# Kernel optimization log

Hardware: AMD Instinct MI355X
Metric: run time of the kernel (lower is better)

Reference implementation:

```python
import jax, jax.numpy as jnp
import numpy as np

WS = 8          # window size
SS = 4          # shift size
NH = 4          # num heads
DIM = 128
RPE_HID = 512
MLP_HID = 512   # 4 * DIM
EPS = 1e-5


def _rel_coords_table(ws):
    h = np.arange(-(ws - 1), ws, dtype=np.float32)
    tbl = np.stack(np.meshgrid(h, h, indexing='ij'), axis=-1)  # [2ws-1, 2ws-1, 2]
    tbl = tbl / (ws - 1) * 8.0
    tbl = np.sign(tbl) * np.log2(np.abs(tbl) + 1.0) / np.log2(8.0)
    return jnp.asarray(tbl, dtype=jnp.float32)


def _rel_pos_index(ws):
    coords = np.stack(np.meshgrid(np.arange(ws), np.arange(ws), indexing='ij'))  # [2, ws, ws]
    cf = coords.reshape(2, -1)
    rel = (cf[:, :, None] - cf[:, None, :]).transpose(1, 2, 0).astype(np.int64)  # [N, N, 2]
    rel[..., 0] += ws - 1
    rel[..., 1] += ws - 1
    rel[..., 0] *= 2 * ws - 1
    return jnp.asarray(rel.sum(-1))  # [N, N]


def _attn_mask(H, W, ws, ss):
    img = np.zeros((H, W), np.float32)
    cnt = 0
    for hsl in (slice(0, -ws), slice(-ws, -ss), slice(-ss, None)):
        for wsl in (slice(0, -ws), slice(-ws, -ss), slice(-ss, None)):
            img[hsl, wsl] = cnt
            cnt += 1
    mw = img.reshape(H // ws, ws, W // ws, ws).transpose(0, 2, 1, 3).reshape(-1, ws * ws)
    diff = mw[:, None, :] - mw[:, :, None]
    return jnp.asarray(np.where(diff != 0, -100.0, 0.0).astype(np.float32))  # [nW, N, N]


def _layernorm(x, w, b):
    mu = x.mean(-1, keepdims=True)
    var = ((x - mu) ** 2).mean(-1, keepdims=True)
    return (x - mu) * jax.lax.rsqrt(var + EPS) * w + b


def setup_inputs() -> dict:
    key = jax.random.key(0)
    ks = jax.random.split(key, 16)
    s = 0.02
    return {
        'x': jax.random.normal(ks[0], (32, 4096, DIM), jnp.float32),
        'qkv_w': jax.random.normal(ks[1], (3 * DIM, DIM), jnp.float32) * s,
        'qkv_b': jnp.zeros((3 * DIM,), jnp.float32),
        'proj_w': jax.random.normal(ks[2], (DIM, DIM), jnp.float32) * s,
        'proj_b': jnp.zeros((DIM,), jnp.float32),
        'rpe_w1': jax.random.normal(ks[3], (RPE_HID, 2), jnp.float32) * s,
        'rpe_b1': jnp.zeros((RPE_HID,), jnp.float32),
        'rpe_w2': jax.random.normal(ks[4], (NH, RPE_HID), jnp.float32) * s,
        'norm1_w': jnp.ones((DIM,), jnp.float32),
        'norm1_b': jnp.zeros((DIM,), jnp.float32),
        'fc1_w': jax.random.normal(ks[5], (MLP_HID, DIM), jnp.float32) * s,
        'fc1_b': jnp.zeros((MLP_HID,), jnp.float32),
        'fc2_w': jax.random.normal(ks[6], (DIM, MLP_HID), jnp.float32) * s,
        'fc2_b': jnp.zeros((DIM,), jnp.float32),
        'norm2_w': jnp.ones((DIM,), jnp.float32),
        'norm2_b': jnp.zeros((DIM,), jnp.float32),
        'H': 64,
        'W': 64,
    }


def reference(x, qkv_w, qkv_b, proj_w, proj_b, rpe_w1, rpe_b1, rpe_w2,
              norm1_w, norm1_b, fc1_w, fc1_b, fc2_w, fc2_b, norm2_w, norm2_b, H, W):
    B, L, C = x.shape
    N = WS * WS
    hd = C // NH
    scale = hd ** -0.5
    nWh, nWw = H // WS, W // WS
    nW = nWh * nWw

    # ---- shifted window partition ----
    xs = x.reshape(B, H, W, C)
    xs = jnp.roll(xs, shift=(-SS, -SS), axis=(1, 2))
    xw = xs.reshape(B, nWh, WS, nWw, WS, C).transpose(0, 1, 3, 2, 4, 5).reshape(-1, N, C)

    # ---- window attention ----
    qkv = xw @ qkv_w.T + qkv_b                              # [B*nW, N, 3C]
    qkv = qkv.reshape(-1, N, 3, NH, hd).transpose(2, 0, 3, 1, 4)
    q, k, v = qkv[0], qkv[1], qkv[2]                        # [B*nW, NH, N, hd]
    attn = jnp.einsum('whnd,whmd->whnm', q * scale, k)      # [B*nW, NH, N, N]

    # continuous relative position bias via MLP on log-spaced coords
    tbl = _rel_coords_table(WS)                             # [2ws-1, 2ws-1, 2]
    t = jax.nn.relu(tbl @ rpe_w1.T + rpe_b1) @ rpe_w2.T     # [2ws-1, 2ws-1, NH]
    t = t.reshape(-1, NH)
    rel_idx = _rel_pos_index(WS)                            # [N, N]
    bias = t[rel_idx].transpose(2, 0, 1)                    # [NH, N, N]
    attn = attn + bias[None]

    # shift mask
    mask = _attn_mask(H, W, WS, SS)                         # [nW, N, N]
    attn = attn.reshape(B, nW, NH, N, N) + mask[None, :, None]
    attn = jax.nn.softmax(attn, axis=-1).reshape(-1, NH, N, N)

    out = jnp.einsum('whnm,whmd->whnd', attn, v)            # [B*nW, NH, N, hd]
    out = out.transpose(0, 2, 1, 3).reshape(-1, N, C)
    out = out @ proj_w.T + proj_b

    # ---- window reverse + unshift ----
    out = out.reshape(B, nWh, nWw, WS, WS, C).transpose(0, 1, 3, 2, 4, 5).reshape(B, H, W, C)
    out = jnp.roll(out, shift=(SS, SS), axis=(1, 2)).reshape(B, L, C)

    # ---- post-norm residual ----
    x = x + _layernorm(out, norm1_w, norm1_b)

    # ---- MLP (GELU exact) + post-norm residual ----
    h = jax.nn.gelu(x @ fc1_w.T + fc1_b, approximate=False)
    h = h @ fc2_w.T + fc2_b
    x = x + _layernorm(h, norm2_w, norm2_b)
    return x
```

## Files before the change

### kernel.cpp

```cpp
#include <hip/hip_runtime.h>
#include <hip/hip_bf16.h>

typedef __attribute__((ext_vector_type(8))) short short8_t;
typedef __attribute__((ext_vector_type(4))) float f32x4_t;
typedef __attribute__((ext_vector_type(2))) float f32x2_t;

#define NHEAD 4
#define SCALE 0.17677669529663687f

#define OFF_W    0L
#define OFF_TBL  393216L
#define OFF_QKV  458752L
#define OFF_H    458752L
#define OFF_ATTN 101122048L
#define OFF_X1BF 134676480L

__device__ __forceinline__ unsigned short f2bf(float f){
  unsigned int u = __float_as_uint(f);
  u += 0x7FFFu + ((u >> 16) & 1u);
  return (unsigned short)(u >> 16);
}
__device__ __forceinline__ float bf2f(unsigned short s){
  return __uint_as_float(((unsigned int)s) << 16);
}

__device__ __forceinline__ int win_row_to_orig(int r){
  int win = r >> 6, n = r & 63;
  int b = win >> 6, wh = (win >> 3) & 7, ww = win & 7;
  int hs = wh*8 + (n >> 3), wsv = ww*8 + (n & 7);
  return (b << 12) + (((hs + 4) & 63) << 6) + ((wsv + 4) & 63);
}

__device__ __forceinline__ float gelu_exact(float x){
  float z  = x * 0.70710678118654752f;
  float az = fabsf(z);
  float t  = __builtin_amdgcn_rcpf(1.0f + 0.3275911f * az);
  float poly = t*(0.254829592f + t*(-0.284496736f + t*(1.421413741f +
               t*(-1.453152027f + t*1.061405429f))));
  float er = 1.0f - poly * __expf(-z*z);
  er = (z < 0.f) ? -er : er;
  return 0.5f * x * (1.0f + er);
}

__global__ __launch_bounds__(256) void prep_kernel(
    const float* __restrict__ qkv_w, const float* __restrict__ proj_w,
    const float* __restrict__ fc1_w, const float* __restrict__ fc2_w,
    const float* __restrict__ rpe_w1, const float* __restrict__ rpe_b1,
    const float* __restrict__ rpe_w2,
    unsigned short* __restrict__ wbf, float* __restrict__ tbl)
{
  if (blockIdx.x == 0) {
    int t = threadIdx.x;
    if (t < 225) {
      int a = t / 15, b = t % 15;
      float v0 = (float)(a - 7) * (8.0f / 7.0f);
      float v1 = (float)(b - 7) * (8.0f / 7.0f);
      float c0 = (v0 > 0.f ? 1.f : (v0 < 0.f ? -1.f : 0.f)) * log2f(fabsf(v0) + 1.f) * (1.0f/3.0f);
      float c1 = (v1 > 0.f ? 1.f : (v1 < 0.f ? -1.f : 0.f)) * log2f(fabsf(v1) + 1.f) * (1.0f/3.0f);
      float a0 = 0.f, a1 = 0.f, a2 = 0.f, a3 = 0.f;
      for (int k = 0; k < 512; k++){
        float h = c0 * rpe_w1[2*k] + c1 * rpe_w1[2*k+1] + rpe_b1[k];
        h = fmaxf(h, 0.f);
        a0 += h * rpe_w2[k];
        a1 += h * rpe_w2[512 + k];
        a2 += h * rpe_w2[1024 + k];
        a3 += h * rpe_w2[1536 + k];
      }
      tbl[t] = a0; tbl[225 + t] = a1; tbl[450 + t] = a2; tbl[675 + t] = a3;
    }
  } else {
    int e = (blockIdx.x - 1) * 256 + threadIdx.x;
    float v;
    if (e < 49152)       v = qkv_w[e];
    else if (e < 65536)  v = proj_w[e - 49152];
    else if (e < 131072) v = fc1_w[e - 65536];
    else                 v = fc2_w[e - 131072];
    wbf[e] = f2bf(v);
  }
}

template<int N, int AMODE, int EPI>
__global__ __launch_bounds__(256) void gemm_a_kernel(
    const void* __restrict__ Ap, const unsigned short* __restrict__ Bw,
    const float* __restrict__ bias, unsigned short* __restrict__ Out)
{
  constexpr int K  = 128;
  constexpr int NC = N / 32;
  int lane = threadIdx.x & 63;
  int wave = threadIdx.x >> 6;
  int l15 = lane & 15, kg = lane >> 4;
  int m0 = (blockIdx.x * 4 + wave) * 64;

  short8_t a[4][4];
#pragma unroll
  for (int mr = 0; mr < 4; mr++){
    int r = m0 + mr*16 + l15;
    if (AMODE == 1) r = win_row_to_orig(r);
    if (AMODE == 2){
      const unsigned short* ap = (const unsigned short*)Ap + (long)r * K + kg * 8;
#pragma unroll
      for (int kc = 0; kc < 4; kc++)
        a[mr][kc] = *(const short8_t*)(ap + kc * 32);
    } else {
      const float* ap = (const float*)Ap + (long)r * K + kg * 8;
#pragma unroll
      for (int kc = 0; kc < 4; kc++){
        f32x4_t a0 = *(const f32x4_t*)(ap + kc * 32);
        f32x4_t a1 = *(const f32x4_t*)(ap + kc * 32 + 4);
        union { short8_t v; unsigned short u[8]; } pk;
        pk.u[0] = f2bf(a0[0]); pk.u[1] = f2bf(a0[1]); pk.u[2] = f2bf(a0[2]); pk.u[3] = f2bf(a0[3]);
        pk.u[4] = f2bf(a1[0]); pk.u[5] = f2bf(a1[1]); pk.u[6] = f2bf(a1[2]); pk.u[7] = f2bf(a1[3]);
        a[mr][kc] = pk.v;
      }
    }
  }

  const unsigned short* bp0 = Bw + (long)l15 * K + kg * 8;

#pragma unroll 2
  for (int nc = 0; nc < NC; nc++){
    short8_t b[2][4];
#pragma unroll
    for (int nr = 0; nr < 2; nr++)
#pragma unroll
      for (int kc = 0; kc < 4; kc++)
        b[nr][kc] = *(const short8_t*)(bp0 + (long)(nc*32 + nr*16) * K + kc * 32);

    f32x4_t acc[4][2];
#pragma unroll
    for (int mr = 0; mr < 4; mr++)
#pragma unroll
      for (int nr = 0; nr < 2; nr++) acc[mr][nr] = (f32x4_t){0.f,0.f,0.f,0.f};
#pragma unroll
    for (int kc = 0; kc < 4; kc++)
#pragma unroll
      for (int mr = 0; mr < 4; mr++)
#pragma unroll
        for (int nr = 0; nr < 2; nr++)
          acc[mr][nr] = __builtin_amdgcn_mfma_f32_16x16x32_bf16(a[mr][kc], b[nr][kc], acc[mr][nr], 0, 0, 0);

#pragma unroll
    for (int nr = 0; nr < 2; nr++){
      int col = nc*32 + nr*16 + l15;
      float bv = bias[col];
#pragma unroll
      for (int mr = 0; mr < 4; mr++)
#pragma unroll
        for (int i = 0; i < 4; i++){
          float v = acc[mr][nr][i] + bv;
          if (EPI == 2) v = gelu_exact(v);
          Out[(long)(m0 + mr*16 + kg*4 + i) * N + col] = f2bf(v);
        }
    }
  }
}

template<int K, int SCATTER, int RESBF, int OUTBF>
__global__ __launch_bounds__(256) void gemm_b_ln_kernel(
    const unsigned short* __restrict__ Ap, const unsigned short* __restrict__ Bw,
    const float* __restrict__ bias,
    const float* __restrict__ lnw, const float* __restrict__ lnb,
    const void* __restrict__ Res, void* __restrict__ OutP)
{
  constexpr int KC = K / 32;
  int lane = threadIdx.x & 63;
  int wave = threadIdx.x >> 6;
  int l15 = lane & 15, kg = lane >> 4;
  int m0 = (blockIdx.x * 4 + wave) * 32;

  f32x4_t acc[2][8];
#pragma unroll
  for (int mr = 0; mr < 2; mr++)
#pragma unroll
    for (int nt = 0; nt < 8; nt++) acc[mr][nt] = (f32x4_t){0.f,0.f,0.f,0.f};

  const unsigned short* ap0 = Ap + (long)(m0 + l15) * K + kg * 8;
  const unsigned short* bp0 = Bw + (long)l15 * K + kg * 8;

#pragma unroll 2
  for (int kc = 0; kc < KC; kc++){
    short8_t a0 = *(const short8_t*)(ap0 + kc * 32);
    short8_t a1 = *(const short8_t*)(ap0 + 16 * K + kc * 32);
    short8_t b[8];
#pragma unroll
    for (int nt = 0; nt < 8; nt++)
      b[nt] = *(const short8_t*)(bp0 + (long)nt * 16 * K + kc * 32);
#pragma unroll
    for (int nt = 0; nt < 8; nt++)
      acc[0][nt] = __builtin_amdgcn_mfma_f32_16x16x32_bf16(a0, b[nt], acc[0][nt], 0, 0, 0);
#pragma unroll
    for (int nt = 0; nt < 8; nt++)
      acc[1][nt] = __builtin_amdgcn_mfma_f32_16x16x32_bf16(a1, b[nt], acc[1][nt], 0, 0, 0);
  }

  float bv[8], wv[8], bb[8];
#pragma unroll
  for (int nt = 0; nt < 8; nt++){
    int col = nt*16 + l15;
    bv[nt] = bias[col]; wv[nt] = lnw[col]; bb[nt] = lnb[col];
  }

#pragma unroll
  for (int mr = 0; mr < 2; mr++)
#pragma unroll
    for (int i = 0; i < 4; i++){
      float v[8];
      float s1 = 0.f, s2 = 0.f;
#pragma unroll
      for (int nt = 0; nt < 8; nt++){
        v[nt] = acc[mr][nt][i] + bv[nt];
        s1 += v[nt]; s2 += v[nt]*v[nt];
      }
      s1 += __shfl_xor(s1, 1); s2 += __shfl_xor(s2, 1);
      s1 += __shfl_xor(s1, 2); s2 += __shfl_xor(s2, 2);
      s1 += __shfl_xor(s1, 4); s2 += __shfl_xor(s2, 4);
      s1 += __shfl_xor(s1, 8); s2 += __shfl_xor(s2, 8);
      float mu = s1 * 0.0078125f;
      float var = s2 * 0.0078125f - mu * mu;
      float rs = rsqrtf(var + 1e-5f);
      int row = m0 + mr*16 + kg*4 + i;
      int orow = SCATTER ? win_row_to_orig(row) : row;
      long rb = (long)orow * 128;
#pragma unroll
      for (int nt = 0; nt < 8; nt++){
        int col = nt*16 + l15;
        float r = RESBF ? bf2f(((const unsigned short*)Res)[rb + col])
                        : ((const float*)Res)[rb + col];
        float o = r + (v[nt] - mu) * rs * wv[nt] + bb[nt];
        if (OUTBF) ((unsigned short*)OutP)[rb + col] = f2bf(o);
        else       ((float*)OutP)[rb + col] = o;
      }
    }
}

__global__ __launch_bounds__(256) void attn_kernel(
    const unsigned short* __restrict__ qkv, const float* __restrict__ tbl,
    unsigned short* __restrict__ outp)
{
  __shared__ __align__(16) unsigned short vt[NHEAD][32][72];
  __shared__ __align__(16) unsigned short pl[NHEAD][16][72];
  __shared__ float tl[900];
  int win  = blockIdx.x;
  int head = threadIdx.x >> 6;
  int lane = threadIdx.x & 63;
  int l15 = lane & 15, kg = lane >> 4;

  for (int e = threadIdx.x; e < 900; e += 256) tl[e] = tbl[e];

  const unsigned short* qbase = qkv + (long)win * 64 * 384;

  {
    const unsigned short* vp = qbase + lane * 384 + 256 + head * 32;
#pragma unroll
    for (int d0 = 0; d0 < 4; d0++){
      union { short8_t v; unsigned short u[8]; } pk;
      pk.v = *(const short8_t*)(vp + d0 * 8);
#pragma unroll
      for (int j = 0; j < 8; j++)
        vt[head][d0 * 8 + j][lane] = pk.u[j];
    }
  }

  short8_t kf[4];
#pragma unroll
  for (int nt = 0; nt < 4; nt++)
    kf[nt] = *(const short8_t*)(qbase + (nt * 16 + l15) * 384 + 128 + head * 32 + kg * 8);

  __syncthreads();

  short8_t bvf[2][2];
#pragma unroll
  for (int dt = 0; dt < 2; dt++)
#pragma unroll
    for (int ks = 0; ks < 2; ks++)
      bvf[dt][ks] = *(const short8_t*)(&vt[head][dt * 16 + l15][ks * 32 + kg * 8]);

  const float* tlh = tl + head * 225;
  bool wh7 = ((win >> 3) & 7) == 7;
  bool ww7 = (win & 7) == 7;
  bool crq_lt = (kg & 1) == 0;
  bool crm_lt = (l15 & 7) < 4;
  int  t3m_lo = l15 >> 3;
  int  dj0 = (kg & 1) * 4 - (l15 & 7) + 7;

#pragma unroll
  for (int mt = 0; mt < 4; mt++){
    short8_t qf = *(const short8_t*)(qbase + (mt * 16 + l15) * 384 + head * 32 + kg * 8);
    f32x4_t sacc[4];
#pragma unroll
    for (int nt = 0; nt < 4; nt++)
      sacc[nt] = __builtin_amdgcn_mfma_f32_16x16x32_bf16(qf, kf[nt], (f32x4_t){0.f,0.f,0.f,0.f}, 0, 0, 0);

    int t3q = mt * 2 + (kg >> 1);
    bool rrq_lt = t3q < 4;
    float p[4][4];
#pragma unroll
    for (int nt = 0; nt < 4; nt++){
      int t3m = nt * 2 + t3m_lo;
      const float* bp = tlh + (t3q - t3m + 7) * 15 + dj0;
      bool masked = (wh7 && (rrq_lt != (t3m < 4))) || (ww7 && (crq_lt != crm_lt));
      float mterm = masked ? -100.f : 0.f;
#pragma unroll
      for (int ii = 0; ii < 4; ii++){
        float s = sacc[nt][ii] * SCALE + bp[ii] + mterm;
        p[nt][ii] = __expf(s);
      }
    }
    float inv[4];
#pragma unroll
    for (int ii = 0; ii < 4; ii++){
      float sm = (p[0][ii] + p[1][ii]) + (p[2][ii] + p[3][ii]);
      sm += __shfl_xor(sm, 1); sm += __shfl_xor(sm, 2);
      sm += __shfl_xor(sm, 4); sm += __shfl_xor(sm, 8);
      inv[ii] = 1.f / sm;
    }
#pragma unroll
    for (int nt = 0; nt < 4; nt++)
#pragma unroll
      for (int ii = 0; ii < 4; ii++)
        pl[head][kg * 4 + ii][nt * 16 + l15] = f2bf(p[nt][ii]);

    asm volatile("s_waitcnt lgkmcnt(0)" ::: "memory");

    f32x4_t oacc[2] = {{0.f,0.f,0.f,0.f},{0.f,0.f,0.f,0.f}};
#pragma unroll
    for (int ks = 0; ks < 2; ks++){
      short8_t pa = *(const short8_t*)(&pl[head][l15][ks * 32 + kg * 8]);
#pragma unroll
      for (int dt = 0; dt < 2; dt++)
        oacc[dt] = __builtin_amdgcn_mfma_f32_16x16x32_bf16(pa, bvf[dt][ks], oacc[dt], 0, 0, 0);
    }

    unsigned short* op = outp + ((long)(win * 64 + mt * 16 + kg * 4)) * 128 + head * 32;
#pragma unroll
    for (int ii = 0; ii < 4; ii++)
#pragma unroll
      for (int dt = 0; dt < 2; dt++)
        op[ii * 128 + dt * 16 + l15] = f2bf(oacc[dt][ii] * inv[ii]);
  }
}

extern "C" void kernel_launch(void* const* d_in, const int* in_sizes, int n_in,
                              void* d_out, int out_size, void* d_ws, size_t ws_size,
                              hipStream_t stream)
{
  (void)in_sizes; (void)n_in; (void)out_size; (void)ws_size;
  const float* x      = (const float*)d_in[0];
  const float* qkv_w  = (const float*)d_in[1];
  const float* qkv_b  = (const float*)d_in[2];
  const float* proj_w = (const float*)d_in[3];
  const float* proj_b = (const float*)d_in[4];
  const float* rpe_w1 = (const float*)d_in[5];
  const float* rpe_b1 = (const float*)d_in[6];
  const float* rpe_w2 = (const float*)d_in[7];
  const float* n1w    = (const float*)d_in[8];
  const float* n1b    = (const float*)d_in[9];
  const float* fc1_w  = (const float*)d_in[10];
  const float* fc1_b  = (const float*)d_in[11];
  const float* fc2_w  = (const float*)d_in[12];
  const float* fc2_b  = (const float*)d_in[13];
  const float* n2w    = (const float*)d_in[14];
  const float* n2b    = (const float*)d_in[15];

  char* ws = (char*)d_ws;
  unsigned short* Wbf   = (unsigned short*)(ws + OFF_W);
  float*          tblp  = (float*)(ws + OFF_TBL);
  unsigned short* qkvp  = (unsigned short*)(ws + OFF_QKV);
  unsigned short* attnp = (unsigned short*)(ws + OFF_ATTN);
  unsigned short* x1bf  = (unsigned short*)(ws + OFF_X1BF);
  unsigned short* hp    = (unsigned short*)(ws + OFF_H);

  prep_kernel<<<769, 256, 0, stream>>>(qkv_w, proj_w, fc1_w, fc2_w, rpe_w1, rpe_b1, rpe_w2, Wbf, tblp);
  gemm_a_kernel<384, 1, 0><<<512, 256, 0, stream>>>(x, Wbf, qkv_b, qkvp);
  attn_kernel<<<2048, 256, 0, stream>>>(qkvp, tblp, attnp);
  gemm_b_ln_kernel<128, 1, 0, 1><<<1024, 256, 0, stream>>>(
      attnp, Wbf + 49152, proj_b, n1w, n1b, x, x1bf);
  gemm_a_kernel<512, 2, 2><<<512, 256, 0, stream>>>(x1bf, Wbf + 65536, fc1_b, hp);
  gemm_b_ln_kernel<512, 0, 1, 0><<<1024, 256, 0, stream>>>(
      hp, Wbf + 131072, fc2_b, n2w, n2b, x1bf, d_out);
}
```

Before: 438.4 us.

## Fuse fc1+GELU and fc2+LayerNorm into one MLP kernel keeping hidden in LDS

Replaces the separate fc1 GEMM (writing the 512-wide bf16 hidden activation to global memory) and the fc2+LayerNorm GEMM with a single kernel. Each 64-row block computes fc1 with GELU, stores the hidden tile in XOR-swizzled shared memory, then runs fc2 from LDS with a fused bias, LayerNorm and residual epilogue. This removes the round trip of the large hidden tensor through HBM and one launch. In exchange it uses 64 KB of LDS per block, which limits occupancy, and each block reloads the W2 weights from global/L2.

```diff
diff --git a/kernel.cpp b/kernel.cpp
--- a/kernel.cpp
+++ b/kernel.cpp
@@ -11,7 +11,6 @@
 #define OFF_W    0L
 #define OFF_TBL  393216L
 #define OFF_QKV  458752L
-#define OFF_H    458752L
 #define OFF_ATTN 101122048L
 #define OFF_X1BF 134676480L
 
@@ -233,6 +232,120 @@
     }
 }
 
+__global__ __launch_bounds__(256) void fused_mlp_kernel(
+    const unsigned short* __restrict__ x1, const unsigned short* __restrict__ W1,
+    const float* __restrict__ b1, const unsigned short* __restrict__ W2,
+    const float* __restrict__ b2,
+    const float* __restrict__ lnw, const float* __restrict__ lnb,
+    float* __restrict__ out)
+{
+  __shared__ __align__(16) unsigned short hl[64 * 512];
+  int lane = threadIdx.x & 63;
+  int wave = threadIdx.x >> 6;
+  int l15 = lane & 15, kg = lane >> 4;
+  int m0 = blockIdx.x * 64;
+
+  short8_t a[4][4];
+#pragma unroll
+  for (int mr = 0; mr < 4; mr++){
+    const unsigned short* ap = x1 + (long)(m0 + mr*16 + l15) * 128 + kg * 8;
+#pragma unroll
+    for (int kc = 0; kc < 4; kc++)
+      a[mr][kc] = *(const short8_t*)(ap + kc * 32);
+  }
+
+#pragma unroll
+  for (int nc = 0; nc < 2; nc++){
+    short8_t b[4][4];
+#pragma unroll
+    for (int nr = 0; nr < 4; nr++){
+      const unsigned short* bp = W1 + (long)(wave*128 + nc*64 + nr*16 + l15) * 128 + kg * 8;
+#pragma unroll
+      for (int kc = 0; kc < 4; kc++)
+        b[nr][kc] = *(const short8_t*)(bp + kc * 32);
+    }
+    f32x4_t acc[4][4];
+#pragma unroll
+    for (int mr = 0; mr < 4; mr++)
+#pragma unroll
+      for (int nr = 0; nr < 4; nr++) acc[mr][nr] = (f32x4_t){0.f,0.f,0.f,0.f};
+#pragma unroll
+    for (int kc = 0; kc < 4; kc++)
+#pragma unroll
+      for (int mr = 0; mr < 4; mr++)
+#pragma unroll
+        for (int nr = 0; nr < 4; nr++)
+          acc[mr][nr] = __builtin_amdgcn_mfma_f32_16x16x32_bf16(a[mr][kc], b[nr][kc], acc[mr][nr], 0, 0, 0);
+
+#pragma unroll
+    for (int nr = 0; nr < 4; nr++){
+      int col = wave*128 + nc*64 + nr*16 + l15;
+      float bv = b1[col];
+      int gbase = col >> 3, glo = col & 7;
+#pragma unroll
+      for (int mr = 0; mr < 4; mr++)
+#pragma unroll
+        for (int i = 0; i < 4; i++){
+          int row = mr*16 + kg*4 + i;
+          float v = gelu_exact(acc[mr][nr][i] + bv);
+          hl[row * 512 + ((gbase ^ (row & 7)) << 3) + glo] = f2bf(v);
+        }
+    }
+  }
+  __syncthreads();
+
+  f32x4_t acc2[8];
+#pragma unroll
+  for (int nt = 0; nt < 8; nt++) acc2[nt] = (f32x4_t){0.f,0.f,0.f,0.f};
+
+  int r = wave*16 + l15;
+  const unsigned short* hrow = hl + r * 512;
+
+#pragma unroll 2
+  for (int kc = 0; kc < 16; kc++){
+    int g = (kc*4 + kg) ^ (l15 & 7);
+    short8_t a2 = *(const short8_t*)(hrow + (g << 3));
+    short8_t bb[8];
+#pragma unroll
+    for (int nt = 0; nt < 8; nt++)
+      bb[nt] = *(const short8_t*)(W2 + (long)(nt*16 + l15) * 512 + kc*32 + kg*8);
+#pragma unroll
+    for (int nt = 0; nt < 8; nt++)
+      acc2[nt] = __builtin_amdgcn_mfma_f32_16x16x32_bf16(a2, bb[nt], acc2[nt], 0, 0, 0);
+  }
+
+  float bv[8], wv[8], bbv[8];
+#pragma unroll
+  for (int nt = 0; nt < 8; nt++){
+    int col = nt*16 + l15;
+    bv[nt] = b2[col]; wv[nt] = lnw[col]; bbv[nt] = lnb[col];
+  }
+#pragma unroll
+  for (int i = 0; i < 4; i++){
+    float v[8];
+    float s1 = 0.f, s2 = 0.f;
+#pragma unroll
+    for (int nt = 0; nt < 8; nt++){
+      v[nt] = acc2[nt][i] + bv[nt];
+      s1 += v[nt]; s2 += v[nt]*v[nt];
+    }
+    s1 += __shfl_xor(s1, 1); s2 += __shfl_xor(s2, 1);
+    s1 += __shfl_xor(s1, 2); s2 += __shfl_xor(s2, 2);
+    s1 += __shfl_xor(s1, 4); s2 += __shfl_xor(s2, 4);
+    s1 += __shfl_xor(s1, 8); s2 += __shfl_xor(s2, 8);
+    float mu = s1 * 0.0078125f;
+    float var = s2 * 0.0078125f - mu * mu;
+    float rs = rsqrtf(var + 1e-5f);
+    long rb = (long)(m0 + wave*16 + kg*4 + i) * 128;
+#pragma unroll
+    for (int nt = 0; nt < 8; nt++){
+      int col = nt*16 + l15;
+      float res = bf2f(x1[rb + col]);
+      out[rb + col] = res + (v[nt] - mu) * rs * wv[nt] + bbv[nt];
+    }
+  }
+}
+
 __global__ __launch_bounds__(256) void attn_kernel(
     const unsigned short* __restrict__ qkv, const float* __restrict__ tbl,
     unsigned short* __restrict__ outp)
@@ -368,14 +481,12 @@
   unsigned short* qkvp  = (unsigned short*)(ws + OFF_QKV);
   unsigned short* attnp = (unsigned short*)(ws + OFF_ATTN);
   unsigned short* x1bf  = (unsigned short*)(ws + OFF_X1BF);
-  unsigned short* hp    = (unsigned short*)(ws + OFF_H);
 
   prep_kernel<<<769, 256, 0, stream>>>(qkv_w, proj_w, fc1_w, fc2_w, rpe_w1, rpe_b1, rpe_w2, Wbf, tblp);
   gemm_a_kernel<384, 1, 0><<<512, 256, 0, stream>>>(x, Wbf, qkv_b, qkvp);
   attn_kernel<<<2048, 256, 0, stream>>>(qkvp, tblp, attnp);
   gemm_b_ln_kernel<128, 1, 0, 1><<<1024, 256, 0, stream>>>(
       attnp, Wbf + 49152, proj_b, n1w, n1b, x, x1bf);
-  gemm_a_kernel<512, 2, 2><<<512, 256, 0, stream>>>(x1bf, Wbf + 65536, fc1_b, hp);
-  gemm_b_ln_kernel<512, 0, 1, 0><<<1024, 256, 0, stream>>>(
-      hp, Wbf + 131072, fc2_b, n2w, n2b, x1bf, d_out);
-}
+  fused_mlp_kernel<<<2048, 256, 0, stream>>>(
+      x1bf, Wbf + 65536, fc1_b, Wbf + 131072, fc2_b, n2w, n2b, (float*)d_out);
+}
```

Measured after the change: 500.1 us. 1.14x slower.
